# Optimization experiments

Hardware: AMD Instinct MI355X
Metric: run time of the kernel (lower is better)

## Reference

```python
import jax, jax.numpy as jnp
import numpy as np

DIM = 256
RES = 64
HEADS = 8
WS = 8            # window_size
CS = (8, 64)      # cross_size (cs1 == W so cross grid broadcasts against window grid)
HEAD_DIM = DIM // HEADS
SCALE = HEAD_DIM ** -0.5


def _partition(x, B, sh, sw):
    # x: [B, L, C] -> [B*heads, H//sh, W//sw, sh*sw, head_dim]
    H = W = RES
    C = DIM
    x = x.reshape(B, H // sh, sh, W // sw, sw, HEADS, HEAD_DIM)
    x = x.transpose(0, 5, 1, 3, 2, 4, 6)
    return x.reshape(B * HEADS, H // sh, W // sw, sh * sw, HEAD_DIM)


def setup_inputs() -> dict:
    key = jax.random.key(0)
    qkv = jax.random.normal(key, (3, 8, RES * RES, DIM), dtype=jnp.float32)
    return {"qkv": qkv}


def reference(qkv) -> jnp.ndarray:
    q, k, v = qkv[0], qkv[1], qkv[2]
    B, L, C = q.shape
    H = W = RES

    qw = _partition(q, B, WS, WS) * SCALE            # [Bh, H/ws, W/ws, ws*ws, hd]
    kc = _partition(k, B, CS[0], CS[1])              # [Bh, H/cs0, 1, cs0*cs1, hd]
    vc = _partition(v, B, CS[0], CS[1])

    # Original einsum 'bhwnc,bqkmc->bhwnm' sums k over its cross-window grid (q,k axes);
    # equivalently pre-sum k over those axes, then contract over head_dim.
    k_sum = kc.sum(axis=(1, 2))                      # [Bh, m, hd]
    attn = jnp.einsum('bhwnc,bmc->bhwnm', qw, k_sum) # [Bh, H/ws, W/ws, n, m]
    attn = jax.nn.softmax(attn, axis=-1)

    # broadcast matmul: vc's cross grid (H/cs0, 1) broadcasts to (H/ws, W/ws)
    x = attn @ vc                                    # [Bh, H/ws, W/ws, n, hd]

    x = x.reshape(B, HEADS, H // WS, W // WS, WS, WS, HEAD_DIM)
    x = x.transpose(0, 2, 4, 3, 5, 1, 6).reshape(B, H, W, C).reshape(B, -1, C)
    return x
```

## Files before the change

kernel.cpp:

```cpp
#include <hip/hip_runtime.h>
#include <hip/hip_bf16.h>

#define NB 8
#define L_TOT 4096
#define DIM 256
#define HEADS 8
#define HEAD_DIM 32
#define M_TOT 512
#define QSCALE (0.17677669529663687f * 1.4426950408889634f)

typedef float f32x16 __attribute__((ext_vector_type(16)));
typedef short bf16x8 __attribute__((ext_vector_type(8)));

union BF8 { bf16x8 v; unsigned u[4]; uint2 u2[2]; uint4 u4; };

__device__ __forceinline__ unsigned cvt2(float lo, float hi) {
    __hip_bfloat162 h = __float22bfloat162_rn(make_float2(lo, hi));
    union { __hip_bfloat162 h2; unsigned u; } un;
    un.h2 = h;
    return un.u;
}

__global__ __launch_bounds__(256) void ksum_kernel(const float* __restrict__ k,
                                                   unsigned short* __restrict__ ks) {
    const int blk = blockIdx.x;
    const int bh = blk >> 4, part = blk & 15;
    const int b = bh >> 3, head = bh & 7;
    const float* kb = k + (size_t)b * L_TOT * DIM + head * HEAD_DIM;
    const int c0 = (threadIdx.x & 7) * 4;
    const int m = part * 32 + (threadIdx.x >> 3);
    float4 s = make_float4(0.f, 0.f, 0.f, 0.f);
#pragma unroll
    for (int hq = 0; hq < 8; ++hq) {
        const float4 f = *(const float4*)(kb + (size_t)(hq * 512 + m) * DIM + c0);
        s.x += f.x; s.y += f.y; s.z += f.z; s.w += f.w;
    }
    uint2 o;
    o.x = cvt2(s.x, s.y);
    o.y = cvt2(s.z, s.w);
    const int lane = (m & 31) + 32 * ((c0 >> 3) & 1);
    const size_t off = (size_t)bh * 16384 + (size_t)(m >> 5) * 1024 +
                       (c0 >= 16 ? 512 : 0) + lane * 8 + (c0 & 7);
    *(uint2*)(ks + off) = o;
}

template <bool USE_WS>
__global__ __launch_bounds__(512, 4) void attn_kernel(const float* __restrict__ q,
                                                      const float* __restrict__ kg,
                                                      const float* __restrict__ v,
                                                      const unsigned short* __restrict__ ks,
                                                      float* __restrict__ out) {
    constexpr int KSF_OFF = 16384;
    constexpr int INV_OFF = 32768;
    __shared__ unsigned short smem[33280];
    unsigned short* vF = smem;
    unsigned short* ksF = smem + KSF_OFF;

    const int tid = threadIdx.x;
    const int wave = tid >> 6;
    const int lane = tid & 63;
    const int ql = lane & 31;
    const int hi = lane >> 5;

    const int bid = blockIdx.x;
    const int wk = (bid & 7) * 64 + (bid >> 3);
    const int bh = wk >> 3, h = wk & 7;
    const int b = bh >> 3, head = bh & 7;

    if (USE_WS) {
        const uint4* ksrc4 = (const uint4*)(ks + (size_t)bh * 16384);
        uint4* kdst4 = (uint4*)ksF;
        const uint4 t0 = ksrc4[tid], t1 = ksrc4[512 + tid];
        const uint4 t2 = ksrc4[1024 + tid], t3 = ksrc4[1536 + tid];
        kdst4[tid] = t0; kdst4[512 + tid] = t1;
        kdst4[1024 + tid] = t2; kdst4[1536 + tid] = t3;
    } else {
        const float* kb = kg + (size_t)b * L_TOT * DIM + head * HEAD_DIM;
#pragma unroll
        for (int it = 0; it < 8; ++it) {
            const int idx = it * 512 + tid;
            const int m = idx >> 3, c0 = (idx & 7) * 4;
            float4 s = make_float4(0.f, 0.f, 0.f, 0.f);
#pragma unroll
            for (int hq = 0; hq < 8; ++hq) {
                const float4 f = *(const float4*)(kb + (size_t)(hq * 512 + m) * DIM + c0);
                s.x += f.x; s.y += f.y; s.z += f.z; s.w += f.w;
            }
            uint2 o; o.x = cvt2(s.x, s.y); o.y = cvt2(s.z, s.w);
            const int ln = (m & 31) + 32 * ((c0 >> 3) & 1);
            *(uint2*)(ksF + (m >> 5) * 1024 + (c0 >= 16 ? 512 : 0) + ln * 8 + (c0 & 7)) = o;
        }
    }

    const float* vbase = v + ((size_t)b * L_TOT + h * M_TOT) * DIM + head * HEAD_DIM;
#pragma unroll
    for (int it = 0; it < 8; ++it) {
        const int idx = it * 512 + tid;
        const int m = idx >> 3, c0 = (idx & 7) * 4;
        const float4 f = *(const float4*)(vbase + (size_t)m * DIM + c0);
        const unsigned w0 = cvt2(f.x, f.y), w1 = cvt2(f.z, f.w);
        unsigned short* bp = vF + (m >> 5) * 1024 + ((m >> 4) & 1) * 512 +
                             (c0 + 32 * ((m >> 3) & 1)) * 8 + (m & 7);
        bp[0]  = (unsigned short)w0;
        bp[8]  = (unsigned short)(w0 >> 16);
        bp[16] = (unsigned short)w1;
        bp[24] = (unsigned short)(w1 >> 16);
    }
    __syncthreads();

    const unsigned short* ksW = ksF + lane * 8;
    const unsigned short* vfW = vF + lane * 8;
    float* invW = (float*)(smem + INV_OFF) + wave * 32;
    const float* qbase = q + (size_t)b * L_TOT * DIM + head * HEAD_DIM;

    for (int gi = 0; gi < 2; ++gi) {
        const int wcol = wave, n0 = gi * 32;
        const int n = n0 + ql;
        const int Lq = (h * 8 + (n >> 3)) * 64 + wcol * 8 + (n & 7);
        const float* qp = qbase + (size_t)Lq * DIM;

        BF8 qf0, qf1;
        {
            const float4 f0 = *(const float4*)(qp + 8 * hi);
            const float4 f1 = *(const float4*)(qp + 8 * hi + 4);
            qf0.u[0] = cvt2(f0.x * QSCALE, f0.y * QSCALE);
            qf0.u[1] = cvt2(f0.z * QSCALE, f0.w * QSCALE);
            qf0.u[2] = cvt2(f1.x * QSCALE, f1.y * QSCALE);
            qf0.u[3] = cvt2(f1.z * QSCALE, f1.w * QSCALE);
            const float4 f2 = *(const float4*)(qp + 16 + 8 * hi);
            const float4 f3 = *(const float4*)(qp + 16 + 8 * hi + 4);
            qf1.u[0] = cvt2(f2.x * QSCALE, f2.y * QSCALE);
            qf1.u[1] = cvt2(f2.z * QSCALE, f2.w * QSCALE);
            qf1.u[2] = cvt2(f3.x * QSCALE, f3.y * QSCALE);
            qf1.u[3] = cvt2(f3.z * QSCALE, f3.w * QSCALE);
        }

        f32x16 O;
#pragma unroll
        for (int r = 0; r < 16; ++r) O[r] = 0.f;
        float lsum = 0.f;

        auto qk = [&](int ch) -> f32x16 {
            BF8 A0, A1;
            A0.u4 = *(const uint4*)(ksW + ch * 1024);
            A1.u4 = *(const uint4*)(ksW + ch * 1024 + 512);
            f32x16 z;
#pragma unroll
            for (int r = 0; r < 16; ++r) z[r] = 0.f;
            f32x16 S = __builtin_amdgcn_mfma_f32_32x32x16_bf16(A0.v, qf0.v, z, 0, 0, 0);
            return __builtin_amdgcn_mfma_f32_32x32x16_bf16(A1.v, qf1.v, S, 0, 0, 0);
        };

        auto smPV = [&](const f32x16& S, int ch) {
            BF8 VB0, VB1;
            VB0.u4 = *(const uint4*)(vfW + ch * 1024);
            VB1.u4 = *(const uint4*)(vfW + ch * 1024 + 512);
            float p[16];
#pragma unroll
            for (int r = 0; r < 16; ++r) p[r] = __builtin_amdgcn_exp2f(S[r]);
            const float s0 = (p[0] + p[1]) + (p[2] + p[3]);
            const float s1 = (p[4] + p[5]) + (p[6] + p[7]);
            const float s2 = (p[8] + p[9]) + (p[10] + p[11]);
            const float s3 = (p[12] + p[13]) + (p[14] + p[15]);
            lsum += (s0 + s1) + (s2 + s3);

            unsigned w0 = cvt2(p[0], p[1]),   w1 = cvt2(p[2], p[3]);
            unsigned w2 = cvt2(p[4], p[5]),   w3 = cvt2(p[6], p[7]);
            unsigned w4 = cvt2(p[8], p[9]),   w5 = cvt2(p[10], p[11]);
            unsigned w6 = cvt2(p[12], p[13]), w7 = cvt2(p[14], p[15]);
            asm("v_permlane32_swap_b32 %0, %1" : "+v"(w0), "+v"(w2));
            asm("v_permlane32_swap_b32 %0, %1" : "+v"(w1), "+v"(w3));
            asm("v_permlane32_swap_b32 %0, %1" : "+v"(w4), "+v"(w6));
            asm("v_permlane32_swap_b32 %0, %1" : "+v"(w5), "+v"(w7));
            BF8 PA0, PA1;
            PA0.u[0] = w0; PA0.u[1] = w1; PA0.u[2] = w2; PA0.u[3] = w3;
            PA1.u[0] = w4; PA1.u[1] = w5; PA1.u[2] = w6; PA1.u[3] = w7;
            O = __builtin_amdgcn_mfma_f32_32x32x16_bf16(PA0.v, VB0.v, O, 0, 0, 0);
            O = __builtin_amdgcn_mfma_f32_32x32x16_bf16(PA1.v, VB1.v, O, 0, 0, 0);
        };

        f32x16 Sc = qk(0);
        for (int ch = 0; ch < 15; ++ch) {
            f32x16 Sn = qk(ch + 1);
            smPV(Sc, ch);
            Sc = Sn;
        }
        smPV(Sc, 15);

        lsum += __shfl_xor(lsum, 32, 64);
        const float inv = __builtin_amdgcn_rcpf(lsum);
        if (hi == 0) invW[ql] = inv;

        const int rowBase = h * 512 + (n0 >> 3) * 64 + wcol * 8 + 4 * hi;
        float* ob = out + ((size_t)b * L_TOT + rowBase) * DIM + head * HEAD_DIM + ql;
#pragma unroll
        for (int t = 0; t < 4; ++t) {
            const float4 iv = *(const float4*)(invW + 8 * t + 4 * hi);
            ob[(size_t)(t * 64 + 0) * DIM] = O[4 * t + 0] * iv.x;
            ob[(size_t)(t * 64 + 1) * DIM] = O[4 * t + 1] * iv.y;
            ob[(size_t)(t * 64 + 2) * DIM] = O[4 * t + 2] * iv.z;
            ob[(size_t)(t * 64 + 3) * DIM] = O[4 * t + 3] * iv.w;
        }
    }
}

extern "C" void kernel_launch(void* const* d_in, const int* in_sizes, int n_in,
                              void* d_out, int out_size, void* d_ws, size_t ws_size,
                              hipStream_t stream) {
    const float* qkv = (const float*)d_in[0];
    const float* q = qkv;
    const float* k = qkv + (size_t)NB * L_TOT * DIM;
    const float* v = qkv + (size_t)2 * NB * L_TOT * DIM;
    float* out = (float*)d_out;
    const size_t ks_bytes = (size_t)NB * HEADS * M_TOT * HEAD_DIM * 2;
    if (ws_size >= ks_bytes) {
        unsigned short* ks = (unsigned short*)d_ws;
        ksum_kernel<<<dim3(1024), dim3(256), 0, stream>>>(k, ks);
        attn_kernel<true><<<dim3(512), dim3(512), 0, stream>>>(q, k, v, ks, out);
    } else {
        attn_kernel<false><<<dim3(512), dim3(512), 0, stream>>>(q, k, v, nullptr, out);
    }
}
```

Baseline: 174.2 us.

## Process both query groups per wave in one pass sharing K/V fragments

Merges the two sequential 32-query passes into a single loop over key chunks. Each K-sum and V fragment loaded from LDS now feeds both query groups, and the two independent QK/softmax/PV chains interleave to hide MFMA latency. This halves LDS reads for K and V. In exchange each thread holds two accumulators and two sets of Q fragments, which raises VGPR pressure under the 512-thread, 4-block launch bound and could cause spills.

```diff
diff --git a/kernel.cpp b/kernel.cpp
--- a/kernel.cpp
+++ b/kernel.cpp
@@ -52,7 +52,7 @@
                                                       float* __restrict__ out) {
     constexpr int KSF_OFF = 16384;
     constexpr int INV_OFF = 32768;
-    __shared__ unsigned short smem[33280];
+    __shared__ unsigned short smem[32768 + 8 * 64 * 2];
     unsigned short* vF = smem;
     unsigned short* ksF = smem + KSF_OFF;
 
@@ -110,97 +110,121 @@
 
     const unsigned short* ksW = ksF + lane * 8;
     const unsigned short* vfW = vF + lane * 8;
-    float* invW = (float*)(smem + INV_OFF) + wave * 32;
+    float* invW = (float*)(smem + INV_OFF) + wave * 64;
     const float* qbase = q + (size_t)b * L_TOT * DIM + head * HEAD_DIM;
 
-    for (int gi = 0; gi < 2; ++gi) {
-        const int wcol = wave, n0 = gi * 32;
-        const int n = n0 + ql;
-        const int Lq = (h * 8 + (n >> 3)) * 64 + wcol * 8 + (n & 7);
-        const float* qp = qbase + (size_t)Lq * DIM;
-
-        BF8 qf0, qf1;
-        {
-            const float4 f0 = *(const float4*)(qp + 8 * hi);
-            const float4 f1 = *(const float4*)(qp + 8 * hi + 4);
-            qf0.u[0] = cvt2(f0.x * QSCALE, f0.y * QSCALE);
-            qf0.u[1] = cvt2(f0.z * QSCALE, f0.w * QSCALE);
-            qf0.u[2] = cvt2(f1.x * QSCALE, f1.y * QSCALE);
-            qf0.u[3] = cvt2(f1.z * QSCALE, f1.w * QSCALE);
-            const float4 f2 = *(const float4*)(qp + 16 + 8 * hi);
-            const float4 f3 = *(const float4*)(qp + 16 + 8 * hi + 4);
-            qf1.u[0] = cvt2(f2.x * QSCALE, f2.y * QSCALE);
-            qf1.u[1] = cvt2(f2.z * QSCALE, f2.w * QSCALE);
-            qf1.u[2] = cvt2(f3.x * QSCALE, f3.y * QSCALE);
-            qf1.u[3] = cvt2(f3.z * QSCALE, f3.w * QSCALE);
-        }
-
-        f32x16 O;
-#pragma unroll
-        for (int r = 0; r < 16; ++r) O[r] = 0.f;
-        float lsum = 0.f;
-
-        auto qk = [&](int ch) -> f32x16 {
-            BF8 A0, A1;
-            A0.u4 = *(const uint4*)(ksW + ch * 1024);
-            A1.u4 = *(const uint4*)(ksW + ch * 1024 + 512);
-            f32x16 z;
-#pragma unroll
-            for (int r = 0; r < 16; ++r) z[r] = 0.f;
-            f32x16 S = __builtin_amdgcn_mfma_f32_32x32x16_bf16(A0.v, qf0.v, z, 0, 0, 0);
-            return __builtin_amdgcn_mfma_f32_32x32x16_bf16(A1.v, qf1.v, S, 0, 0, 0);
-        };
-
-        auto smPV = [&](const f32x16& S, int ch) {
-            BF8 VB0, VB1;
-            VB0.u4 = *(const uint4*)(vfW + ch * 1024);
-            VB1.u4 = *(const uint4*)(vfW + ch * 1024 + 512);
-            float p[16];
-#pragma unroll
-            for (int r = 0; r < 16; ++r) p[r] = __builtin_amdgcn_exp2f(S[r]);
-            const float s0 = (p[0] + p[1]) + (p[2] + p[3]);
-            const float s1 = (p[4] + p[5]) + (p[6] + p[7]);
-            const float s2 = (p[8] + p[9]) + (p[10] + p[11]);
-            const float s3 = (p[12] + p[13]) + (p[14] + p[15]);
-            lsum += (s0 + s1) + (s2 + s3);
-
-            unsigned w0 = cvt2(p[0], p[1]),   w1 = cvt2(p[2], p[3]);
-            unsigned w2 = cvt2(p[4], p[5]),   w3 = cvt2(p[6], p[7]);
-            unsigned w4 = cvt2(p[8], p[9]),   w5 = cvt2(p[10], p[11]);
-            unsigned w6 = cvt2(p[12], p[13]), w7 = cvt2(p[14], p[15]);
-            asm("v_permlane32_swap_b32 %0, %1" : "+v"(w0), "+v"(w2));
-            asm("v_permlane32_swap_b32 %0, %1" : "+v"(w1), "+v"(w3));
-            asm("v_permlane32_swap_b32 %0, %1" : "+v"(w4), "+v"(w6));
-            asm("v_permlane32_swap_b32 %0, %1" : "+v"(w5), "+v"(w7));
-            BF8 PA0, PA1;
-            PA0.u[0] = w0; PA0.u[1] = w1; PA0.u[2] = w2; PA0.u[3] = w3;
-            PA1.u[0] = w4; PA1.u[1] = w5; PA1.u[2] = w6; PA1.u[3] = w7;
-            O = __builtin_amdgcn_mfma_f32_32x32x16_bf16(PA0.v, VB0.v, O, 0, 0, 0);
-            O = __builtin_amdgcn_mfma_f32_32x32x16_bf16(PA1.v, VB1.v, O, 0, 0, 0);
-        };
-
-        f32x16 Sc = qk(0);
-        for (int ch = 0; ch < 15; ++ch) {
-            f32x16 Sn = qk(ch + 1);
-            smPV(Sc, ch);
-            Sc = Sn;
-        }
-        smPV(Sc, 15);
-
-        lsum += __shfl_xor(lsum, 32, 64);
-        const float inv = __builtin_amdgcn_rcpf(lsum);
-        if (hi == 0) invW[ql] = inv;
-
-        const int rowBase = h * 512 + (n0 >> 3) * 64 + wcol * 8 + 4 * hi;
-        float* ob = out + ((size_t)b * L_TOT + rowBase) * DIM + head * HEAD_DIM + ql;
-#pragma unroll
-        for (int t = 0; t < 4; ++t) {
-            const float4 iv = *(const float4*)(invW + 8 * t + 4 * hi);
-            ob[(size_t)(t * 64 + 0) * DIM] = O[4 * t + 0] * iv.x;
-            ob[(size_t)(t * 64 + 1) * DIM] = O[4 * t + 1] * iv.y;
-            ob[(size_t)(t * 64 + 2) * DIM] = O[4 * t + 2] * iv.z;
-            ob[(size_t)(t * 64 + 3) * DIM] = O[4 * t + 3] * iv.w;
-        }
+    const int wcol = wave;
+    const int na = ql, nb = 32 + ql;
+    const int Lqa = (h * 8 + (na >> 3)) * 64 + wcol * 8 + (na & 7);
+    const int Lqb = (h * 8 + (nb >> 3)) * 64 + wcol * 8 + (nb & 7);
+
+    BF8 qfa0, qfa1, qfb0, qfb1;
+    {
+        const float* qp = qbase + (size_t)Lqa * DIM;
+        const float4 f0 = *(const float4*)(qp + 8 * hi);
+        const float4 f1 = *(const float4*)(qp + 8 * hi + 4);
+        qfa0.u[0] = cvt2(f0.x * QSCALE, f0.y * QSCALE);
+        qfa0.u[1] = cvt2(f0.z * QSCALE, f0.w * QSCALE);
+        qfa0.u[2] = cvt2(f1.x * QSCALE, f1.y * QSCALE);
+        qfa0.u[3] = cvt2(f1.z * QSCALE, f1.w * QSCALE);
+        const float4 f2 = *(const float4*)(qp + 16 + 8 * hi);
+        const float4 f3 = *(const float4*)(qp + 16 + 8 * hi + 4);
+        qfa1.u[0] = cvt2(f2.x * QSCALE, f2.y * QSCALE);
+        qfa1.u[1] = cvt2(f2.z * QSCALE, f2.w * QSCALE);
+        qfa1.u[2] = cvt2(f3.x * QSCALE, f3.y * QSCALE);
+        qfa1.u[3] = cvt2(f3.z * QSCALE, f3.w * QSCALE);
+    }
+    {
+        const float* qp = qbase + (size_t)Lqb * DIM;
+        const float4 f0 = *(const float4*)(qp + 8 * hi);
+        const float4 f1 = *(const float4*)(qp + 8 * hi + 4);
+        qfb0.u[0] = cvt2(f0.x * QSCALE, f0.y * QSCALE);
+        qfb0.u[1] = cvt2(f0.z * QSCALE, f0.w * QSCALE);
+        qfb0.u[2] = cvt2(f1.x * QSCALE, f1.y * QSCALE);
+        qfb0.u[3] = cvt2(f1.z * QSCALE, f1.w * QSCALE);
+        const float4 f2 = *(const float4*)(qp + 16 + 8 * hi);
+        const float4 f3 = *(const float4*)(qp + 16 + 8 * hi + 4);
+        qfb1.u[0] = cvt2(f2.x * QSCALE, f2.y * QSCALE);
+        qfb1.u[1] = cvt2(f2.z * QSCALE, f2.w * QSCALE);
+        qfb1.u[2] = cvt2(f3.x * QSCALE, f3.y * QSCALE);
+        qfb1.u[3] = cvt2(f3.z * QSCALE, f3.w * QSCALE);
+    }
+
+    f32x16 Oa, Ob;
+#pragma unroll
+    for (int r = 0; r < 16; ++r) { Oa[r] = 0.f; Ob[r] = 0.f; }
+    float lsa = 0.f, lsb = 0.f;
+
+    auto smPV = [&](const f32x16& S, const BF8& VB0, const BF8& VB1,
+                    float& lsum, f32x16& O) {
+        float p[16];
+#pragma unroll
+        for (int r = 0; r < 16; ++r) p[r] = __builtin_amdgcn_exp2f(S[r]);
+        const float s0 = (p[0] + p[1]) + (p[2] + p[3]);
+        const float s1 = (p[4] + p[5]) + (p[6] + p[7]);
+        const float s2 = (p[8] + p[9]) + (p[10] + p[11]);
+        const float s3 = (p[12] + p[13]) + (p[14] + p[15]);
+        lsum += (s0 + s1) + (s2 + s3);
+
+        unsigned w0 = cvt2(p[0], p[1]),   w1 = cvt2(p[2], p[3]);
+        unsigned w2 = cvt2(p[4], p[5]),   w3 = cvt2(p[6], p[7]);
+        unsigned w4 = cvt2(p[8], p[9]),   w5 = cvt2(p[10], p[11]);
+        unsigned w6 = cvt2(p[12], p[13]), w7 = cvt2(p[14], p[15]);
+        asm("v_permlane32_swap_b32 %0, %1" : "+v"(w0), "+v"(w2));
+        asm("v_permlane32_swap_b32 %0, %1" : "+v"(w1), "+v"(w3));
+        asm("v_permlane32_swap_b32 %0, %1" : "+v"(w4), "+v"(w6));
+        asm("v_permlane32_swap_b32 %0, %1" : "+v"(w5), "+v"(w7));
+        BF8 PA0, PA1;
+        PA0.u[0] = w0; PA0.u[1] = w1; PA0.u[2] = w2; PA0.u[3] = w3;
+        PA1.u[0] = w4; PA1.u[1] = w5; PA1.u[2] = w6; PA1.u[3] = w7;
+        O = __builtin_amdgcn_mfma_f32_32x32x16_bf16(PA0.v, VB0.v, O, 0, 0, 0);
+        O = __builtin_amdgcn_mfma_f32_32x32x16_bf16(PA1.v, VB1.v, O, 0, 0, 0);
+    };
+
+#pragma unroll 2
+    for (int ch = 0; ch < 16; ++ch) {
+        BF8 A0, A1, VB0, VB1;
+        A0.u4 = *(const uint4*)(ksW + ch * 1024);
+        A1.u4 = *(const uint4*)(ksW + ch * 1024 + 512);
+        VB0.u4 = *(const uint4*)(vfW + ch * 1024);
+        VB1.u4 = *(const uint4*)(vfW + ch * 1024 + 512);
+
+        f32x16 Sa;
+#pragma unroll
+        for (int r = 0; r < 16; ++r) Sa[r] = 0.f;
+        Sa = __builtin_amdgcn_mfma_f32_32x32x16_bf16(A0.v, qfa0.v, Sa, 0, 0, 0);
+        Sa = __builtin_amdgcn_mfma_f32_32x32x16_bf16(A1.v, qfa1.v, Sa, 0, 0, 0);
+        smPV(Sa, VB0, VB1, lsa, Oa);
+
+        f32x16 Sb;
+#pragma unroll
+        for (int r = 0; r < 16; ++r) Sb[r] = 0.f;
+        Sb = __builtin_amdgcn_mfma_f32_32x32x16_bf16(A0.v, qfb0.v, Sb, 0, 0, 0);
+        Sb = __builtin_amdgcn_mfma_f32_32x32x16_bf16(A1.v, qfb1.v, Sb, 0, 0, 0);
+        smPV(Sb, VB0, VB1, lsb, Ob);
+    }
+
+    lsa += __shfl_xor(lsa, 32, 64);
+    lsb += __shfl_xor(lsb, 32, 64);
+    const float inva = __builtin_amdgcn_rcpf(lsa);
+    const float invb = __builtin_amdgcn_rcpf(lsb);
+    if (hi == 0) { invW[ql] = inva; invW[32 + ql] = invb; }
+
+    const int rowBase = h * 512 + wcol * 8 + 4 * hi;
+    float* oa = out + ((size_t)b * L_TOT + rowBase) * DIM + head * HEAD_DIM + ql;
+    float* ob = oa + (size_t)256 * DIM;
+#pragma unroll
+    for (int t = 0; t < 4; ++t) {
+        const float4 iva = *(const float4*)(invW + 8 * t + 4 * hi);
+        const float4 ivb = *(const float4*)(invW + 32 + 8 * t + 4 * hi);
+        oa[(size_t)(t * 64 + 0) * DIM] = Oa[4 * t + 0] * iva.x;
+        oa[(size_t)(t * 64 + 1) * DIM] = Oa[4 * t + 1] * iva.y;
+        oa[(size_t)(t * 64 + 2) * DIM] = Oa[4 * t + 2] * iva.z;
+        oa[(size_t)(t * 64 + 3) * DIM] = Oa[4 * t + 3] * iva.w;
+        ob[(size_t)(t * 64 + 0) * DIM] = Ob[4 * t + 0] * ivb.x;
+        ob[(size_t)(t * 64 + 1) * DIM] = Ob[4 * t + 1] * ivb.y;
+        ob[(size_t)(t * 64 + 2) * DIM] = Ob[4 * t + 2] * ivb.z;
+        ob[(size_t)(t * 64 + 3) * DIM] = Ob[4 * t + 3] * ivb.w;
     }
 }
 
```

New measurement: 176.3 us. No clear change (+1.2%).

## Switch attention to 16x16x32 MFMA tiles with 1024-thread blocks

Applied to the files above, without the earlier changes.

Replaces the 32x32x16 MFMA formulation with 16x16x32 bf16 MFMAs, so each wave processes 16 query rows per group. The block grows to 1024 threads (16 waves), and the k-sum and V shared-memory layouts are re-swizzled to match the new operand fragments. The permlane swaps for the P operand go away, and the software pipelining of QK against PV is replaced by a fully unrolled loop. The aim is more waves in flight per CU and less per-wave register pressure, at the cost of more, smaller MFMA instructions and more shared-memory fragment reads per unit of work.

```diff
diff --git a/kernel.cpp b/kernel.cpp
--- a/kernel.cpp
+++ b/kernel.cpp
@@ -9,10 +9,10 @@
 #define M_TOT 512
 #define QSCALE (0.17677669529663687f * 1.4426950408889634f)
 
-typedef float f32x16 __attribute__((ext_vector_type(16)));
+typedef float f32x4 __attribute__((ext_vector_type(4)));
 typedef short bf16x8 __attribute__((ext_vector_type(8)));
 
-union BF8 { bf16x8 v; unsigned u[4]; uint2 u2[2]; uint4 u4; };
+union BF8 { bf16x8 v; unsigned u[4]; uint4 u4; };
 
 __device__ __forceinline__ unsigned cvt2(float lo, float hi) {
     __hip_bfloat162 h = __float22bfloat162_rn(make_float2(lo, hi));
@@ -38,29 +38,27 @@
     uint2 o;
     o.x = cvt2(s.x, s.y);
     o.y = cvt2(s.z, s.w);
-    const int lane = (m & 31) + 32 * ((c0 >> 3) & 1);
-    const size_t off = (size_t)bh * 16384 + (size_t)(m >> 5) * 1024 +
-                       (c0 >= 16 ? 512 : 0) + lane * 8 + (c0 & 7);
+    const size_t off = (size_t)bh * 16384 + (m >> 4) * 512 + (m & 15) * 8 +
+                       (c0 >> 3) * 128 + (c0 & 7);
     *(uint2*)(ks + off) = o;
 }
 
 template <bool USE_WS>
-__global__ __launch_bounds__(512, 4) void attn_kernel(const float* __restrict__ q,
-                                                      const float* __restrict__ kg,
-                                                      const float* __restrict__ v,
-                                                      const unsigned short* __restrict__ ks,
-                                                      float* __restrict__ out) {
-    constexpr int KSF_OFF = 16384;
-    constexpr int INV_OFF = 32768;
-    __shared__ unsigned short smem[33280];
-    unsigned short* vF = smem;
-    unsigned short* ksF = smem + KSF_OFF;
+__global__ __launch_bounds__(1024, 8) void attn_kernel(const float* __restrict__ q,
+                                                       const float* __restrict__ kg,
+                                                       const float* __restrict__ v,
+                                                       const unsigned short* __restrict__ ks,
+                                                       float* __restrict__ out) {
+    __shared__ __align__(16) unsigned short smem[32768 + 512];
+    unsigned short* ksF = smem;
+    unsigned short* vF = smem + 16384;
+    float* invAll = (float*)(smem + 32768);
 
     const int tid = threadIdx.x;
     const int wave = tid >> 6;
     const int lane = tid & 63;
-    const int ql = lane & 31;
-    const int hi = lane >> 5;
+    const int l15 = lane & 15;
+    const int g = lane >> 4;
 
     const int bid = blockIdx.x;
     const int wk = (bid & 7) * 64 + (bid >> 3);
@@ -70,15 +68,13 @@
     if (USE_WS) {
         const uint4* ksrc4 = (const uint4*)(ks + (size_t)bh * 16384);
         uint4* kdst4 = (uint4*)ksF;
-        const uint4 t0 = ksrc4[tid], t1 = ksrc4[512 + tid];
-        const uint4 t2 = ksrc4[1024 + tid], t3 = ksrc4[1536 + tid];
-        kdst4[tid] = t0; kdst4[512 + tid] = t1;
-        kdst4[1024 + tid] = t2; kdst4[1536 + tid] = t3;
+        kdst4[tid] = ksrc4[tid];
+        kdst4[1024 + tid] = ksrc4[1024 + tid];
     } else {
         const float* kb = kg + (size_t)b * L_TOT * DIM + head * HEAD_DIM;
 #pragma unroll
-        for (int it = 0; it < 8; ++it) {
-            const int idx = it * 512 + tid;
+        for (int it = 0; it < 4; ++it) {
+            const int idx = it * 1024 + tid;
             const int m = idx >> 3, c0 = (idx & 7) * 4;
             float4 s = make_float4(0.f, 0.f, 0.f, 0.f);
 #pragma unroll
@@ -87,20 +83,22 @@
                 s.x += f.x; s.y += f.y; s.z += f.z; s.w += f.w;
             }
             uint2 o; o.x = cvt2(s.x, s.y); o.y = cvt2(s.z, s.w);
-            const int ln = (m & 31) + 32 * ((c0 >> 3) & 1);
-            *(uint2*)(ksF + (m >> 5) * 1024 + (c0 >= 16 ? 512 : 0) + ln * 8 + (c0 & 7)) = o;
+            *(uint2*)(ksF + (m >> 4) * 512 + (m & 15) * 8 + (c0 >> 3) * 128 + (c0 & 7)) = o;
         }
     }
 
     const float* vbase = v + ((size_t)b * L_TOT + h * M_TOT) * DIM + head * HEAD_DIM;
 #pragma unroll
-    for (int it = 0; it < 8; ++it) {
-        const int idx = it * 512 + tid;
+    for (int it = 0; it < 4; ++it) {
+        const int idx = it * 1024 + tid;
         const int m = idx >> 3, c0 = (idx & 7) * 4;
         const float4 f = *(const float4*)(vbase + (size_t)m * DIM + c0);
         const unsigned w0 = cvt2(f.x, f.y), w1 = cvt2(f.z, f.w);
-        unsigned short* bp = vF + (m >> 5) * 1024 + ((m >> 4) & 1) * 512 +
-                             (c0 + 32 * ((m >> 3) & 1)) * 8 + (m & 7);
+        const int mm = m & 31;
+        const int vg = (mm & 15) >> 2;
+        const int vj = (mm & 3) + (mm >= 16 ? 4 : 0);
+        unsigned short* bp = vF + (2 * (m >> 5) + (c0 >> 4)) * 512 + vj +
+                             (16 * vg + (c0 & 15)) * 8;
         bp[0]  = (unsigned short)w0;
         bp[8]  = (unsigned short)(w0 >> 16);
         bp[16] = (unsigned short)w1;
@@ -110,97 +108,72 @@
 
     const unsigned short* ksW = ksF + lane * 8;
     const unsigned short* vfW = vF + lane * 8;
-    float* invW = (float*)(smem + INV_OFF) + wave * 32;
+    float* invW = invAll + wave * 16;
     const float* qbase = q + (size_t)b * L_TOT * DIM + head * HEAD_DIM;
 
     for (int gi = 0; gi < 2; ++gi) {
-        const int wcol = wave, n0 = gi * 32;
-        const int n = n0 + ql;
-        const int Lq = (h * 8 + (n >> 3)) * 64 + wcol * 8 + (n & 7);
-        const float* qp = qbase + (size_t)Lq * DIM;
+        const int G = wave * 2 + gi;
+        const int wcol = G >> 2, n0 = (G & 3) * 16;
 
-        BF8 qf0, qf1;
+        const int Lq = (h * 8 + (n0 >> 3) + (l15 >> 3)) * 64 + wcol * 8 + (lane & 7);
+        const float* qp = qbase + (size_t)Lq * DIM + 8 * g;
+        BF8 qf;
         {
-            const float4 f0 = *(const float4*)(qp + 8 * hi);
-            const float4 f1 = *(const float4*)(qp + 8 * hi + 4);
-            qf0.u[0] = cvt2(f0.x * QSCALE, f0.y * QSCALE);
-            qf0.u[1] = cvt2(f0.z * QSCALE, f0.w * QSCALE);
-            qf0.u[2] = cvt2(f1.x * QSCALE, f1.y * QSCALE);
-            qf0.u[3] = cvt2(f1.z * QSCALE, f1.w * QSCALE);
-            const float4 f2 = *(const float4*)(qp + 16 + 8 * hi);
-            const float4 f3 = *(const float4*)(qp + 16 + 8 * hi + 4);
-            qf1.u[0] = cvt2(f2.x * QSCALE, f2.y * QSCALE);
-            qf1.u[1] = cvt2(f2.z * QSCALE, f2.w * QSCALE);
-            qf1.u[2] = cvt2(f3.x * QSCALE, f3.y * QSCALE);
-            qf1.u[3] = cvt2(f3.z * QSCALE, f3.w * QSCALE);
+            const float4 f0 = *(const float4*)(qp);
+            const float4 f1 = *(const float4*)(qp + 4);
+            qf.u[0] = cvt2(f0.x * QSCALE, f0.y * QSCALE);
+            qf.u[1] = cvt2(f0.z * QSCALE, f0.w * QSCALE);
+            qf.u[2] = cvt2(f1.x * QSCALE, f1.y * QSCALE);
+            qf.u[3] = cvt2(f1.z * QSCALE, f1.w * QSCALE);
         }
 
-        f32x16 O;
-#pragma unroll
-        for (int r = 0; r < 16; ++r) O[r] = 0.f;
+        f32x4 O0 = {0.f, 0.f, 0.f, 0.f};
+        f32x4 O1 = {0.f, 0.f, 0.f, 0.f};
+        const f32x4 Z = {0.f, 0.f, 0.f, 0.f};
         float lsum = 0.f;
 
-        auto qk = [&](int ch) -> f32x16 {
-            BF8 A0, A1;
-            A0.u4 = *(const uint4*)(ksW + ch * 1024);
-            A1.u4 = *(const uint4*)(ksW + ch * 1024 + 512);
-            f32x16 z;
 #pragma unroll
-            for (int r = 0; r < 16; ++r) z[r] = 0.f;
-            f32x16 S = __builtin_amdgcn_mfma_f32_32x32x16_bf16(A0.v, qf0.v, z, 0, 0, 0);
-            return __builtin_amdgcn_mfma_f32_32x32x16_bf16(A1.v, qf1.v, S, 0, 0, 0);
-        };
-
-        auto smPV = [&](const f32x16& S, int ch) {
-            BF8 VB0, VB1;
+        for (int ch = 0; ch < 16; ++ch) {
+            BF8 A0, A1, VB0, VB1;
+            A0.u4  = *(const uint4*)(ksW + ch * 1024);
+            A1.u4  = *(const uint4*)(ksW + ch * 1024 + 512);
             VB0.u4 = *(const uint4*)(vfW + ch * 1024);
             VB1.u4 = *(const uint4*)(vfW + ch * 1024 + 512);
-            float p[16];
-#pragma unroll
-            for (int r = 0; r < 16; ++r) p[r] = __builtin_amdgcn_exp2f(S[r]);
-            const float s0 = (p[0] + p[1]) + (p[2] + p[3]);
-            const float s1 = (p[4] + p[5]) + (p[6] + p[7]);
-            const float s2 = (p[8] + p[9]) + (p[10] + p[11]);
-            const float s3 = (p[12] + p[13]) + (p[14] + p[15]);
-            lsum += (s0 + s1) + (s2 + s3);
 
-            unsigned w0 = cvt2(p[0], p[1]),   w1 = cvt2(p[2], p[3]);
-            unsigned w2 = cvt2(p[4], p[5]),   w3 = cvt2(p[6], p[7]);
-            unsigned w4 = cvt2(p[8], p[9]),   w5 = cvt2(p[10], p[11]);
-            unsigned w6 = cvt2(p[12], p[13]), w7 = cvt2(p[14], p[15]);
-            asm("v_permlane32_swap_b32 %0, %1" : "+v"(w0), "+v"(w2));
-            asm("v_permlane32_swap_b32 %0, %1" : "+v"(w1), "+v"(w3));
-            asm("v_permlane32_swap_b32 %0, %1" : "+v"(w4), "+v"(w6));
-            asm("v_permlane32_swap_b32 %0, %1" : "+v"(w5), "+v"(w7));
-            BF8 PA0, PA1;
-            PA0.u[0] = w0; PA0.u[1] = w1; PA0.u[2] = w2; PA0.u[3] = w3;
-            PA1.u[0] = w4; PA1.u[1] = w5; PA1.u[2] = w6; PA1.u[3] = w7;
-            O = __builtin_amdgcn_mfma_f32_32x32x16_bf16(PA0.v, VB0.v, O, 0, 0, 0);
-            O = __builtin_amdgcn_mfma_f32_32x32x16_bf16(PA1.v, VB1.v, O, 0, 0, 0);
-        };
+            f32x4 S0 = __builtin_amdgcn_mfma_f32_16x16x32_bf16(A0.v, qf.v, Z, 0, 0, 0);
+            f32x4 S1 = __builtin_amdgcn_mfma_f32_16x16x32_bf16(A1.v, qf.v, Z, 0, 0, 0);
 
-        f32x16 Sc = qk(0);
-        for (int ch = 0; ch < 15; ++ch) {
-            f32x16 Sn = qk(ch + 1);
-            smPV(Sc, ch);
-            Sc = Sn;
+            const float p00 = __builtin_amdgcn_exp2f(S0[0]);
+            const float p01 = __builtin_amdgcn_exp2f(S0[1]);
+            const float p02 = __builtin_amdgcn_exp2f(S0[2]);
+            const float p03 = __builtin_amdgcn_exp2f(S0[3]);
+            const float p10 = __builtin_amdgcn_exp2f(S1[0]);
+            const float p11 = __builtin_amdgcn_exp2f(S1[1]);
+            const float p12 = __builtin_amdgcn_exp2f(S1[2]);
+            const float p13 = __builtin_amdgcn_exp2f(S1[3]);
+            lsum += ((p00 + p01) + (p02 + p03)) + ((p10 + p11) + (p12 + p13));
+
+            BF8 PA;
+            PA.u[0] = cvt2(p00, p01);
+            PA.u[1] = cvt2(p02, p03);
+            PA.u[2] = cvt2(p10, p11);
+            PA.u[3] = cvt2(p12, p13);
+            O0 = __builtin_amdgcn_mfma_f32_16x16x32_bf16(PA.v, VB0.v, O0, 0, 0, 0);
+            O1 = __builtin_amdgcn_mfma_f32_16x16x32_bf16(PA.v, VB1.v, O1, 0, 0, 0);
         }
-        smPV(Sc, 15);
 
+        lsum += __shfl_xor(lsum, 16, 64);
         lsum += __shfl_xor(lsum, 32, 64);
         const float inv = __builtin_amdgcn_rcpf(lsum);
-        if (hi == 0) invW[ql] = inv;
+        if (lane < 16) invW[l15] = inv;
+        const float4 iv = *(const float4*)(invW + 4 * g);
 
-        const int rowBase = h * 512 + (n0 >> 3) * 64 + wcol * 8 + 4 * hi;
-        float* ob = out + ((size_t)b * L_TOT + rowBase) * DIM + head * HEAD_DIM + ql;
-#pragma unroll
-        for (int t = 0; t < 4; ++t) {
-            const float4 iv = *(const float4*)(invW + 8 * t + 4 * hi);
-            ob[(size_t)(t * 64 + 0) * DIM] = O[4 * t + 0] * iv.x;
-            ob[(size_t)(t * 64 + 1) * DIM] = O[4 * t + 1] * iv.y;
-            ob[(size_t)(t * 64 + 2) * DIM] = O[4 * t + 2] * iv.z;
-            ob[(size_t)(t * 64 + 3) * DIM] = O[4 * t + 3] * iv.w;
-        }
+        const int rowL = (h * 8 + (n0 >> 3) + (g >> 1)) * 64 + wcol * 8 + ((4 * g) & 7);
+        float* ob = out + ((size_t)b * L_TOT + rowL) * DIM + head * HEAD_DIM + l15;
+        ob[0 * DIM]      = O0[0] * iv.x;  ob[0 * DIM + 16] = O1[0] * iv.x;
+        ob[1 * DIM]      = O0[1] * iv.y;  ob[1 * DIM + 16] = O1[1] * iv.y;
+        ob[2 * DIM]      = O0[2] * iv.z;  ob[2 * DIM + 16] = O1[2] * iv.z;
+        ob[3 * DIM]      = O0[3] * iv.w;  ob[3 * DIM + 16] = O1[3] * iv.w;
     }
 }
 
@@ -216,8 +189,8 @@
     if (ws_size >= ks_bytes) {
         unsigned short* ks = (unsigned short*)d_ws;
         ksum_kernel<<<dim3(1024), dim3(256), 0, stream>>>(k, ks);
-        attn_kernel<true><<<dim3(512), dim3(512), 0, stream>>>(q, k, v, ks, out);
+        attn_kernel<true><<<dim3(512), dim3(1024), 0, stream>>>(q, k, v, ks, out);
     } else {
-        attn_kernel<false><<<dim3(512), dim3(512), 0, stream>>>(q, k, v, nullptr, out);
+        attn_kernel<false><<<dim3(512), dim3(1024), 0, stream>>>(q, k, v, nullptr, out);
     }
 }
```

New measurement: 433.6 us. 149% more time.
